# Kernel optimization log

Hardware: AMD Instinct MI355X
Metric: run time of the kernel (lower is better)

The kernel has to match this reference:

```python
import jax, jax.numpy as jnp
import numpy as np
from jax import lax

B, S, D, NH, K = 4, 2048, 1024, 16, 3
EPS = 1e-6


def custom_layernorm(x, gamma, beta):
    # torch-style: std with ddof=1, eps added to std (not var)
    mean = jnp.mean(x, axis=-1, keepdims=True)
    var = jnp.sum((x - mean) ** 2, axis=-1, keepdims=True) / (x.shape[-1] - 1)
    std = jnp.sqrt(var)
    return gamma * ((x - mean) / (std + EPS)) + beta


def setup_inputs() -> dict:
    key = jax.random.key(0)
    ks = jax.random.split(key, 10)
    s = 1.0 / np.sqrt(D)
    return {
        "x": jax.random.normal(ks[0], (B, S, D), jnp.float32),
        "Wq": jax.random.normal(ks[1], (D, D), jnp.float32) * s,
        "bq": jax.random.normal(ks[2], (D,), jnp.float32) * 0.02,
        "Wk": jax.random.normal(ks[3], (D, D), jnp.float32) * s,
        "Wv": jax.random.normal(ks[4], (D, D), jnp.float32) * s,
        "bv": jax.random.normal(ks[5], (D,), jnp.float32) * 0.02,
        "conv_w": jax.random.normal(ks[6], (D, D // NH, K), jnp.float32) * (1.0 / np.sqrt((D // NH) * K)),
        "conv_b": jax.random.normal(ks[7], (D,), jnp.float32) * 0.02,
        "gamma": jnp.ones((D,), jnp.float32),
        "beta": jnp.zeros((D,), jnp.float32),
        "Wo": jax.random.normal(ks[8], (D, D), jnp.float32) * s,
        "bo": jax.random.normal(ks[9], (D,), jnp.float32) * 0.02,
    }


def reference(x, Wq, bq, Wk, Wv, bv, conv_w, conv_b, gamma, beta, Wo, bo):
    d = x.shape[-1]
    groups = d // conv_w.shape[1]
    pad = conv_w.shape[2] // 2

    q = x @ Wq + bq
    k = x @ Wk  # key has no bias
    v = x @ Wv + bv

    # grouped conv1d over sequence dim (NCW layout)
    xc = jnp.transpose(x, (0, 2, 1))  # [B, D, S]
    conv_out = lax.conv_general_dilated(
        xc, conv_w, window_strides=(1,), padding=[(pad, pad)],
        feature_group_count=groups,
        dimension_numbers=("NCH", "OIH", "NCH"),
    ) + conv_b[None, :, None]
    conv_out = jnp.transpose(conv_out, (0, 2, 1))  # [B, S, D]
    conv_out = custom_layernorm(conv_out, gamma, beta)  # dropout = identity (eval)

    scale = 1.0 / jnp.sqrt(jnp.asarray(d, x.dtype))
    scores = jnp.einsum("bqd,bkd->bqk", q, k) * scale  # [B, S, S]
    attn = jax.nn.softmax(scores, axis=-1)
    attention_out = jnp.einsum("bqk,bkd->bqd", attn, v)

    combined = custom_layernorm(conv_out + attention_out, gamma, beta)
    return combined @ Wo + bo + x
```

## Files before the change

### kernel.cpp

```cpp
#include <hip/hip_runtime.h>
#include <cstdint>


#define DEV __device__ __forceinline__

typedef unsigned short u16;
typedef __attribute__((ext_vector_type(8))) short bf16x8;
typedef __attribute__((ext_vector_type(4))) float f32x4;

static const int Sn = 2048, Dn = 1024;

DEV float bf2f(u16 u) { union { unsigned int i; float f; } w; w.i = ((unsigned int)u) << 16; return w.f; }
DEV u16 f2bf(float f) {
  union { float f; unsigned int i; } w; w.f = f;
  unsigned int x = w.i;
  return (u16)((x + 0x7FFFu + ((x >> 16) & 1u)) >> 16);
}

DEV void gload_lds16(const u16* gsrc, u16* lds_dst) {
  __builtin_amdgcn_global_load_lds(
      (const __attribute__((address_space(1))) void*)gsrc,
      (__attribute__((address_space(3))) void*)lds_dst,
      16, 0, 0);
}

DEV float block_allreduce_sum(float v, float* red, int tid) {
  #pragma unroll
  for (int o = 32; o > 0; o >>= 1) v += __shfl_down(v, o, 64);
  __syncthreads();
  if ((tid & 63) == 0) red[tid >> 6] = v;
  __syncthreads();
  return red[0] + red[1] + red[2] + red[3];
}

DEV float block_allreduce_max(float v, float* red, int tid) {
  #pragma unroll
  for (int o = 32; o > 0; o >>= 1) v = fmaxf(v, __shfl_down(v, o, 64));
  __syncthreads();
  if ((tid & 63) == 0) red[tid >> 6] = v;
  __syncthreads();
  return fmaxf(fmaxf(red[0], red[1]), fmaxf(red[2], red[3]));
}

__global__ __launch_bounds__(256)
void cvt_f32_bf16(const float* __restrict__ s, u16* __restrict__ d, int n) {
  int i = (blockIdx.x * 256 + threadIdx.x) * 4;
  if (i >= n) return;
  float4 v = *(const float4*)&s[i];
  ushort4 o;
  o.x = f2bf(v.x); o.y = f2bf(v.y); o.z = f2bf(v.z); o.w = f2bf(v.w);
  *(ushort4*)&d[i] = o;
}

__global__ __launch_bounds__(256)
void transpose_cvt4(const float* __restrict__ w0, const float* __restrict__ w1,
                    const float* __restrict__ w2, const float* __restrict__ w3,
                    u16* __restrict__ dst_base) {
  __shared__ u16 sm[64][68];
  int z = blockIdx.z;
  const float* src = (z == 0) ? w0 : (z == 1) ? w1 : (z == 2) ? w2 : w3;
  u16* dst = dst_base + (size_t)z * 1048576u;
  int i0 = blockIdx.y << 6, j0 = blockIdx.x << 6;
  int tid = threadIdx.x, tx = tid & 15, r0 = tid >> 4;
  #pragma unroll
  for (int rr = r0; rr < 64; rr += 16) {
    float4 v = *(const float4*)&src[(long)(i0 + rr) * 1024 + j0 + tx * 4];
    sm[rr][tx*4+0] = f2bf(v.x); sm[rr][tx*4+1] = f2bf(v.y);
    sm[rr][tx*4+2] = f2bf(v.z); sm[rr][tx*4+3] = f2bf(v.w);
  }
  __syncthreads();
  #pragma unroll
  for (int cc = r0; cc < 64; cc += 16) {
    ushort4 o;
    o.x = sm[tx*4+0][cc]; o.y = sm[tx*4+1][cc];
    o.z = sm[tx*4+2][cc]; o.w = sm[tx*4+3][cc];
    *(ushort4*)&dst[(long)(j0 + cc) * 1024 + i0 + tx * 4] = o;
  }
}

__global__ __launch_bounds__(256)
void transpose_u16(const u16* __restrict__ src, u16* __restrict__ dst,
                   int src_ld, int dst_ld, long sbs, long dbs) {
  __shared__ u16 sm[64][68];
  const u16* s = src + (long)blockIdx.z * sbs;
  u16* d = dst + (long)blockIdx.z * dbs;
  int i0 = blockIdx.y << 6, j0 = blockIdx.x << 6;
  int tid = threadIdx.x, tx = tid & 15, r0 = tid >> 4;
  #pragma unroll
  for (int rr = r0; rr < 64; rr += 16) {
    ushort4 v = *(const ushort4*)&s[(long)(i0 + rr) * src_ld + j0 + tx * 4];
    sm[rr][tx*4+0] = v.x; sm[rr][tx*4+1] = v.y; sm[rr][tx*4+2] = v.z; sm[rr][tx*4+3] = v.w;
  }
  __syncthreads();
  #pragma unroll
  for (int cc = r0; cc < 64; cc += 16) {
    ushort4 o;
    o.x = sm[tx*4+0][cc]; o.y = sm[tx*4+1][cc];
    o.z = sm[tx*4+2][cc]; o.w = sm[tx*4+3][cc];
    *(ushort4*)&d[(long)(j0 + cc) * dst_ld + i0 + tx * 4] = o;
  }
}

__global__ void concat_bias(const float* __restrict__ bq, const float* __restrict__ bv,
                            float* __restrict__ qb) {
  int j = blockIdx.x * 256 + threadIdx.x;
  if (j >= 3072) return;
  float v = 0.0f;
  if (j < 1024) v = bq[j];
  else if (j >= 2048) v = bv[j - 2048];
  qb[j] = v;
}

__global__ void conv_w_prep(const float* __restrict__ w, u16* __restrict__ wt) {
  int oc = blockIdx.x;
  int k = threadIdx.x;
  int t = k >> 6, i = k & 63;
  wt[oc * 192 + k] = f2bf(w[oc * 192 + i * 3 + t]);
}

template<typename CT>
__global__ __launch_bounds__(256, 2)
void gemm_nt(const u16* __restrict__ A, const u16* __restrict__ A2, long Abs, int lda,
             const u16* __restrict__ B, long Bbs, int ldb,
             CT* __restrict__ C, CT* __restrict__ C2, long Cbs, int ldc,
             int zsplit, int K, float scale,
             const float* __restrict__ bias, int bias_bs,
             const float* __restrict__ res, long Rbs, int ldr) {
  __shared__ u16 sA[128 * 32];
  __shared__ u16 sB[128 * 32];
  int tid = threadIdx.x;
  int lane = tid & 63, wv = tid >> 6;
  int quad = lane >> 4, lm = lane & 15;
  int wr = wv >> 1, wc = wv & 1;
  long m0 = (long)blockIdx.x * 128, n0 = (long)blockIdx.y * 128;
  int z = blockIdx.z;
  if (z >= zsplit) { A = A2 + (long)(z - zsplit) * Abs; C = C2 + (long)(z - zsplit) * Cbs; }
  else             { A = A  + (long)z * Abs;            C = C  + (long)z * Cbs; }
  B += (long)z * Bbs;
  if (res) res += (long)z * Rbs;

  f32x4 acc[4][4] = {};

  int srow = wv * 16 + (lane >> 2);
  int sch = (lane & 3) * 8;
  const u16* Ap = A + (m0 + srow) * (long)lda + sch;
  const u16* Bp = B + (n0 + srow) * (long)ldb + sch;
  u16* lA = &sA[wv * 16 * 32];
  u16* lB = &sB[wv * 16 * 32];

  for (int k0 = 0; k0 < K; k0 += 32) {
    gload_lds16(Ap + k0, lA);
    gload_lds16(Ap + 64 * (long)lda + k0, lA + 64 * 32);
    gload_lds16(Bp + k0, lB);
    gload_lds16(Bp + 64 * (long)ldb + k0, lB + 64 * 32);
    __syncthreads();
    bf16x8 af[4], bfr[4];
    #pragma unroll
    for (int mi = 0; mi < 4; mi++)
      af[mi] = *(const bf16x8*)&sA[(wr * 64 + mi * 16 + lm) * 32 + quad * 8];
    #pragma unroll
    for (int ni = 0; ni < 4; ni++)
      bfr[ni] = *(const bf16x8*)&sB[(wc * 64 + ni * 16 + lm) * 32 + quad * 8];
    #pragma unroll
    for (int mi = 0; mi < 4; mi++)
      #pragma unroll
      for (int ni = 0; ni < 4; ni++)
        acc[mi][ni] = __builtin_amdgcn_mfma_f32_16x16x32_bf16(af[mi], bfr[ni], acc[mi][ni], 0, 0, 0);
    __syncthreads();
  }

  #pragma unroll
  for (int mi = 0; mi < 4; mi++) {
    #pragma unroll
    for (int ni = 0; ni < 4; ni++) {
      int col = (int)n0 + wc * 64 + ni * 16 + lm;
      float bv = bias ? bias[(long)z * bias_bs + col] : 0.0f;
      #pragma unroll
      for (int r = 0; r < 4; r++) {
        long rowg = m0 + wr * 64 + mi * 16 + quad * 4 + r;
        float v = acc[mi][ni][r] * scale + bv;
        if (res) v += res[rowg * (long)ldr + col];
        if constexpr (sizeof(CT) == 2) C[rowg * (long)ldc + col] = f2bf(v);
        else                           C[rowg * (long)ldc + col] = v;
      }
    }
  }
}

__global__ __launch_bounds__(256)
void conv_mfma(const u16* __restrict__ xb, const u16* __restrict__ wt,
               const float* __restrict__ cb, u16* __restrict__ out) {
  __shared__ u16 sx[130][72];
  int s0 = blockIdx.x * 128;
  int g = blockIdx.y;
  int b = blockIdx.z;
  int tid = threadIdx.x, lane = tid & 63, wv = tid >> 6;
  int quad = lane >> 4, lm = lane & 15;

  for (int idx = tid; idx < 130 * 16; idx += 256) {
    int r = idx >> 4, c4 = (idx & 15) * 4;
    int s = s0 - 1 + r;
    ushort4 v;
    if (s >= 0 && s < Sn) v = *(const ushort4*)&xb[((long)b * Sn + s) * Dn + g * 64 + c4];
    else { v.x = 0; v.y = 0; v.z = 0; v.w = 0; }
    *(ushort4*)&sx[r][c4] = v;
  }
  __syncthreads();

  f32x4 acc[2][4] = {};
  const u16* wg = wt + (long)g * 64 * 192;
  #pragma unroll
  for (int ks = 0; ks < 6; ks++) {
    int t = ks >> 1;
    int i0 = (ks & 1) * 32 + quad * 8;
    bf16x8 a0 = *(const bf16x8*)&sx[wv * 32 + lm + t][i0];
    bf16x8 a1 = *(const bf16x8*)&sx[wv * 32 + 16 + lm + t][i0];
    #pragma unroll
    for (int nf = 0; nf < 4; nf++) {
      bf16x8 bf = *(const bf16x8*)&wg[(nf * 16 + lm) * 192 + ks * 32 + quad * 8];
      acc[0][nf] = __builtin_amdgcn_mfma_f32_16x16x32_bf16(a0, bf, acc[0][nf], 0, 0, 0);
      acc[1][nf] = __builtin_amdgcn_mfma_f32_16x16x32_bf16(a1, bf, acc[1][nf], 0, 0, 0);
    }
  }
  #pragma unroll
  for (int mi = 0; mi < 2; mi++) {
    #pragma unroll
    for (int nf = 0; nf < 4; nf++) {
      int col = g * 64 + nf * 16 + lm;
      float bias = cb[col];
      #pragma unroll
      for (int r = 0; r < 4; r++) {
        int row = wv * 32 + mi * 16 + quad * 4 + r;
        out[((long)b * Sn + s0 + row) * Dn + col] = f2bf(acc[mi][nf][r] + bias);
      }
    }
  }
}

__global__ __launch_bounds__(256)
void ln_kernel(const u16* __restrict__ a, const u16* __restrict__ b2,
               const float* __restrict__ gamma, const float* __restrict__ beta,
               u16* __restrict__ out) {
  __shared__ float red[4];
  long row = blockIdx.x;
  int tid = threadIdx.x;
  long base = row * Dn + tid * 4;
  ushort4 av = *(const ushort4*)&a[base];
  float v0 = bf2f(av.x), v1 = bf2f(av.y), v2 = bf2f(av.z), v3 = bf2f(av.w);
  if (b2) {
    ushort4 bv4 = *(const ushort4*)&b2[base];
    v0 += bf2f(bv4.x); v1 += bf2f(bv4.y); v2 += bf2f(bv4.z); v3 += bf2f(bv4.w);
  }
  float s = block_allreduce_sum(v0 + v1 + v2 + v3, red, tid);
  float mean = s * (1.0f / 1024.0f);
  float d0 = v0 - mean, d1 = v1 - mean, d2 = v2 - mean, d3 = v3 - mean;
  float sq = block_allreduce_sum(d0 * d0 + d1 * d1 + d2 * d2 + d3 * d3, red, tid);
  float inv = 1.0f / (sqrtf(sq * (1.0f / 1023.0f)) + 1e-6f);
  float4 gv = *(const float4*)&gamma[tid * 4];
  float4 bev = *(const float4*)&beta[tid * 4];
  ushort4 o;
  o.x = f2bf(gv.x * d0 * inv + bev.x);
  o.y = f2bf(gv.y * d1 * inv + bev.y);
  o.z = f2bf(gv.z * d2 * inv + bev.z);
  o.w = f2bf(gv.w * d3 * inv + bev.w);
  *(ushort4*)&out[base] = o;
}

__global__ __launch_bounds__(256)
void softmax_bf16(u16* __restrict__ pa, u16* __restrict__ pb, int rowsplit) {
  __shared__ float red[4];
  long row = blockIdx.x;
  u16* p = (row < rowsplit) ? pa + row * 2048 : pb + (row - rowsplit) * 2048;
  int tid = threadIdx.x;
  ushort4 a = *(const ushort4*)&p[tid * 8];
  ushort4 b = *(const ushort4*)&p[tid * 8 + 4];
  float f0 = bf2f(a.x), f1 = bf2f(a.y), f2 = bf2f(a.z), f3 = bf2f(a.w);
  float f4 = bf2f(b.x), f5 = bf2f(b.y), f6 = bf2f(b.z), f7 = bf2f(b.w);
  float m = fmaxf(fmaxf(fmaxf(f0, f1), fmaxf(f2, f3)),
                  fmaxf(fmaxf(f4, f5), fmaxf(f6, f7)));
  m = block_allreduce_max(m, red, tid);
  float e0 = __expf(f0 - m), e1 = __expf(f1 - m), e2 = __expf(f2 - m), e3 = __expf(f3 - m);
  float e4 = __expf(f4 - m), e5 = __expf(f5 - m), e6 = __expf(f6 - m), e7 = __expf(f7 - m);
  float s = block_allreduce_sum(e0 + e1 + e2 + e3 + e4 + e5 + e6 + e7, red, tid);
  float inv = 1.0f / s;
  ushort4 o1, o2;
  o1.x = f2bf(e0 * inv); o1.y = f2bf(e1 * inv); o1.z = f2bf(e2 * inv); o1.w = f2bf(e3 * inv);
  o2.x = f2bf(e4 * inv); o2.y = f2bf(e5 * inv); o2.z = f2bf(e6 * inv); o2.w = f2bf(e7 * inv);
  *(ushort4*)&p[tid * 8] = o1;
  *(ushort4*)&p[tid * 8 + 4] = o2;
}

static const size_t OFF_WT    = 0;
static const size_t OFF_QKVB  = 8ull << 20;
static const size_t OFF_WCONV = (8ull << 20) + (64 << 10);
static const size_t OFF_Q     = 9ull << 20;
static const size_t OFF_K     = 25ull << 20;
static const size_t OFF_V     = 41ull << 20;
static const size_t OFF_PW    = 57ull << 20;

extern "C" void kernel_launch(void* const* d_in, const int* in_sizes, int n_in,
                              void* d_out, int out_size, void* d_ws, size_t ws_size,
                              hipStream_t stream) {
  const float* x     = (const float*)d_in[0];
  const float* Wq    = (const float*)d_in[1];
  const float* bq    = (const float*)d_in[2];
  const float* Wk    = (const float*)d_in[3];
  const float* Wv    = (const float*)d_in[4];
  const float* bv    = (const float*)d_in[5];
  const float* cw    = (const float*)d_in[6];
  const float* cb    = (const float*)d_in[7];
  const float* gamma = (const float*)d_in[8];
  const float* beta  = (const float*)d_in[9];
  const float* Wo    = (const float*)d_in[10];
  const float* bo    = (const float*)d_in[11];
  float* out = (float*)d_out;
  char* ws = (char*)d_ws;

  u16*   wT    = (u16*)(ws + OFF_WT);
  float* qkvb  = (float*)(ws + OFF_QKVB);
  u16*   wconv = (u16*)(ws + OFF_WCONV);
  u16*   Qb    = (u16*)(ws + OFF_Q);
  u16*   Kb    = (u16*)(ws + OFF_K);
  u16*   Vb    = (u16*)(ws + OFF_V);
  u16*   Pw    = (u16*)(ws + OFF_PW);
  u16*   xb    = (u16*)d_out;
  u16*   Pd    = (u16*)d_out;
  u16*   vt    = (u16*)d_out + 8388608;
  u16*   conv  = Vb;
  u16*   attn  = Qb;
  u16*   combined = Kb;
  const long PBS = (long)Sn * Sn;

  dim3 tb(256);

  transpose_cvt4<<<dim3(16, 16, 4), tb, 0, stream>>>(Wq, Wk, Wv, Wo, wT);
  concat_bias<<<dim3(12), tb, 0, stream>>>(bq, bv, qkvb);
  conv_w_prep<<<dim3(1024), dim3(192), 0, stream>>>(cw, wconv);
  cvt_f32_bf16<<<dim3(8192), tb, 0, stream>>>(x, xb, 8388608);

  gemm_nt<u16><<<dim3(64, 8, 3), tb, 0, stream>>>(
      xb, nullptr, 0, 1024, wT, 1048576, 1024, Qb, (u16*)nullptr, 8388608, 1024,
      99, 1024, 1.0f, qkvb, 1024, nullptr, 0, 0);
  transpose_u16<<<dim3(16, 32, 4), tb, 0, stream>>>(
      Vb, vt, 1024, 2048, (long)Sn * Dn, (long)Dn * Sn);
  conv_mfma<<<dim3(16, 16, 4), tb, 0, stream>>>(xb, wconv, cb, conv);
  ln_kernel<<<dim3(8192), tb, 0, stream>>>(conv, nullptr, gamma, beta, conv);

  if (ws_size >= (73ull << 20)) {
    gemm_nt<u16><<<dim3(16, 16, 4), tb, 0, stream>>>(
        Qb, Qb + 2 * (long)Sn * Dn, (long)Sn * Dn, 1024,
        Kb, (long)Sn * Dn, 1024,
        Pd, Pw, PBS, 2048,
        2, 1024, 0.03125f, nullptr, 0, nullptr, 0, 0);
    softmax_bf16<<<dim3(8192), tb, 0, stream>>>(Pd, Pw, 4096);
    gemm_nt<u16><<<dim3(16, 8, 4), tb, 0, stream>>>(
        Pd, Pw, PBS, 2048,
        vt, (long)Dn * Sn, 2048,
        attn, attn + 2 * (long)Sn * Dn, (long)Sn * Dn, 1024,
        2, 2048, 1.0f, nullptr, 0, nullptr, 0, 0);
  } else {
    for (int c = 0; c < 2; c++) {
      long off = (long)c * 2 * Sn * Dn;
      gemm_nt<u16><<<dim3(16, 16, 2), tb, 0, stream>>>(
          Qb + off, nullptr, (long)Sn * Dn, 1024, Kb + off, (long)Sn * Dn, 1024,
          Pd, (u16*)nullptr, PBS, 2048,
          99, 1024, 0.03125f, nullptr, 0, nullptr, 0, 0);
      softmax_bf16<<<dim3(4096), tb, 0, stream>>>(Pd, Pd, 4096);
      gemm_nt<u16><<<dim3(16, 8, 2), tb, 0, stream>>>(
          Pd, nullptr, PBS, 2048, vt + off, (long)Dn * Sn, 2048,
          attn + off, (u16*)nullptr, (long)Sn * Dn, 1024,
          99, 2048, 1.0f, nullptr, 0, nullptr, 0, 0);
    }
  }

  ln_kernel<<<dim3(8192), tb, 0, stream>>>(conv, attn, gamma, beta, combined);
  gemm_nt<float><<<dim3(64, 8, 1), tb, 0, stream>>>(
      combined, nullptr, 0, 1024, wT + 3u * 1048576u, 0, 1024,
      out, (float*)nullptr, 0, 1024,
      99, 1024, 1.0f, bo, 0, x, 0, 1024);
}
```

Baseline: 383.4 us.

## Merge prep kernels, merge conv with V transpose, and load two K-slices per GEMM sync

New measurement: 359.4 us. 1.07x faster.

```diff
diff --git a/kernel.cpp b/kernel.cpp
--- a/kernel.cpp
+++ b/kernel.cpp
@@ -43,79 +43,57 @@
 }
 
 __global__ __launch_bounds__(256)
-void cvt_f32_bf16(const float* __restrict__ s, u16* __restrict__ d, int n) {
-  int i = (blockIdx.x * 256 + threadIdx.x) * 4;
-  if (i >= n) return;
-  float4 v = *(const float4*)&s[i];
-  ushort4 o;
-  o.x = f2bf(v.x); o.y = f2bf(v.y); o.z = f2bf(v.z); o.w = f2bf(v.w);
-  *(ushort4*)&d[i] = o;
-}
-
-__global__ __launch_bounds__(256)
-void transpose_cvt4(const float* __restrict__ w0, const float* __restrict__ w1,
-                    const float* __restrict__ w2, const float* __restrict__ w3,
-                    u16* __restrict__ dst_base) {
+void prep_all(const float* __restrict__ Wq, const float* __restrict__ Wk,
+              const float* __restrict__ Wv, const float* __restrict__ Wo,
+              u16* __restrict__ wT,
+              const float* __restrict__ bq, const float* __restrict__ bv,
+              float* __restrict__ qkvb,
+              const float* __restrict__ cw, u16* __restrict__ wconv,
+              const float* __restrict__ x, u16* __restrict__ xb) {
   __shared__ u16 sm[64][68];
-  int z = blockIdx.z;
-  const float* src = (z == 0) ? w0 : (z == 1) ? w1 : (z == 2) ? w2 : w3;
-  u16* dst = dst_base + (size_t)z * 1048576u;
-  int i0 = blockIdx.y << 6, j0 = blockIdx.x << 6;
-  int tid = threadIdx.x, tx = tid & 15, r0 = tid >> 4;
-  #pragma unroll
-  for (int rr = r0; rr < 64; rr += 16) {
-    float4 v = *(const float4*)&src[(long)(i0 + rr) * 1024 + j0 + tx * 4];
-    sm[rr][tx*4+0] = f2bf(v.x); sm[rr][tx*4+1] = f2bf(v.y);
-    sm[rr][tx*4+2] = f2bf(v.z); sm[rr][tx*4+3] = f2bf(v.w);
-  }
-  __syncthreads();
-  #pragma unroll
-  for (int cc = r0; cc < 64; cc += 16) {
+  int blk = blockIdx.x;
+  int tid = threadIdx.x;
+  if (blk < 1024) {
+    int w = blk >> 8, t = blk & 255;
+    const float* src = (w == 0) ? Wq : (w == 1) ? Wk : (w == 2) ? Wv : Wo;
+    u16* dst = wT + (size_t)w * 1048576u;
+    int i0 = (t >> 4) << 6, j0 = (t & 15) << 6;
+    int tx = tid & 15, r0 = tid >> 4;
+    #pragma unroll
+    for (int rr = r0; rr < 64; rr += 16) {
+      float4 v = *(const float4*)&src[(long)(i0 + rr) * 1024 + j0 + tx * 4];
+      sm[rr][tx*4+0] = f2bf(v.x); sm[rr][tx*4+1] = f2bf(v.y);
+      sm[rr][tx*4+2] = f2bf(v.z); sm[rr][tx*4+3] = f2bf(v.w);
+    }
+    __syncthreads();
+    #pragma unroll
+    for (int cc = r0; cc < 64; cc += 16) {
+      ushort4 o;
+      o.x = sm[tx*4+0][cc]; o.y = sm[tx*4+1][cc];
+      o.z = sm[tx*4+2][cc]; o.w = sm[tx*4+3][cc];
+      *(ushort4*)&dst[(long)(j0 + cc) * 1024 + i0 + tx * 4] = o;
+    }
+  } else if (blk < 1040) {
+    int oc0 = (blk - 1024) * 64;
+    for (int idx = tid; idx < 64 * 192; idx += 256) {
+      int oc = oc0 + idx / 192; int k = idx % 192;
+      int t = k >> 6, i = k & 63;
+      wconv[(long)oc * 192 + k] = f2bf(cw[(long)oc * 192 + i * 3 + t]);
+    }
+  } else if (blk == 1040) {
+    for (int j = tid; j < 3072; j += 256) {
+      float v = 0.0f;
+      if (j < 1024) v = bq[j];
+      else if (j >= 2048) v = bv[j - 2048];
+      qkvb[j] = v;
+    }
+  } else {
+    int i = (blk - 1041) * 1024 + tid * 4;
+    float4 v = *(const float4*)&x[i];
     ushort4 o;
-    o.x = sm[tx*4+0][cc]; o.y = sm[tx*4+1][cc];
-    o.z = sm[tx*4+2][cc]; o.w = sm[tx*4+3][cc];
-    *(ushort4*)&dst[(long)(j0 + cc) * 1024 + i0 + tx * 4] = o;
-  }
-}
-
-__global__ __launch_bounds__(256)
-void transpose_u16(const u16* __restrict__ src, u16* __restrict__ dst,
-                   int src_ld, int dst_ld, long sbs, long dbs) {
-  __shared__ u16 sm[64][68];
-  const u16* s = src + (long)blockIdx.z * sbs;
-  u16* d = dst + (long)blockIdx.z * dbs;
-  int i0 = blockIdx.y << 6, j0 = blockIdx.x << 6;
-  int tid = threadIdx.x, tx = tid & 15, r0 = tid >> 4;
-  #pragma unroll
-  for (int rr = r0; rr < 64; rr += 16) {
-    ushort4 v = *(const ushort4*)&s[(long)(i0 + rr) * src_ld + j0 + tx * 4];
-    sm[rr][tx*4+0] = v.x; sm[rr][tx*4+1] = v.y; sm[rr][tx*4+2] = v.z; sm[rr][tx*4+3] = v.w;
-  }
-  __syncthreads();
-  #pragma unroll
-  for (int cc = r0; cc < 64; cc += 16) {
-    ushort4 o;
-    o.x = sm[tx*4+0][cc]; o.y = sm[tx*4+1][cc];
-    o.z = sm[tx*4+2][cc]; o.w = sm[tx*4+3][cc];
-    *(ushort4*)&d[(long)(j0 + cc) * dst_ld + i0 + tx * 4] = o;
-  }
-}
-
-__global__ void concat_bias(const float* __restrict__ bq, const float* __restrict__ bv,
-                            float* __restrict__ qb) {
-  int j = blockIdx.x * 256 + threadIdx.x;
-  if (j >= 3072) return;
-  float v = 0.0f;
-  if (j < 1024) v = bq[j];
-  else if (j >= 2048) v = bv[j - 2048];
-  qb[j] = v;
-}
-
-__global__ void conv_w_prep(const float* __restrict__ w, u16* __restrict__ wt) {
-  int oc = blockIdx.x;
-  int k = threadIdx.x;
-  int t = k >> 6, i = k & 63;
-  wt[oc * 192 + k] = f2bf(w[oc * 192 + i * 3 + t]);
+    o.x = f2bf(v.x); o.y = f2bf(v.y); o.z = f2bf(v.z); o.w = f2bf(v.w);
+    *(ushort4*)&xb[i] = o;
+  }
 }
 
 template<typename CT>
@@ -126,8 +104,8 @@
              int zsplit, int K, float scale,
              const float* __restrict__ bias, int bias_bs,
              const float* __restrict__ res, long Rbs, int ldr) {
-  __shared__ u16 sA[128 * 32];
-  __shared__ u16 sB[128 * 32];
+  __shared__ u16 sA[2][128 * 32];
+  __shared__ u16 sB[2][128 * 32];
   int tid = threadIdx.x;
   int lane = tid & 63, wv = tid >> 6;
   int quad = lane >> 4, lm = lane & 15;
@@ -145,27 +123,33 @@
   int sch = (lane & 3) * 8;
   const u16* Ap = A + (m0 + srow) * (long)lda + sch;
   const u16* Bp = B + (n0 + srow) * (long)ldb + sch;
-  u16* lA = &sA[wv * 16 * 32];
-  u16* lB = &sB[wv * 16 * 32];
-
-  for (int k0 = 0; k0 < K; k0 += 32) {
-    gload_lds16(Ap + k0, lA);
-    gload_lds16(Ap + 64 * (long)lda + k0, lA + 64 * 32);
-    gload_lds16(Bp + k0, lB);
-    gload_lds16(Bp + 64 * (long)ldb + k0, lB + 64 * 32);
-    __syncthreads();
-    bf16x8 af[4], bfr[4];
-    #pragma unroll
-    for (int mi = 0; mi < 4; mi++)
-      af[mi] = *(const bf16x8*)&sA[(wr * 64 + mi * 16 + lm) * 32 + quad * 8];
-    #pragma unroll
-    for (int ni = 0; ni < 4; ni++)
-      bfr[ni] = *(const bf16x8*)&sB[(wc * 64 + ni * 16 + lm) * 32 + quad * 8];
-    #pragma unroll
-    for (int mi = 0; mi < 4; mi++)
+  const int lofs = wv * 16 * 32;
+
+  for (int k0 = 0; k0 < K; k0 += 64) {
+    #pragma unroll
+    for (int h = 0; h < 2; h++) {
+      int kh = k0 + h * 32;
+      gload_lds16(Ap + kh, &sA[h][lofs]);
+      gload_lds16(Ap + 64 * (long)lda + kh, &sA[h][lofs + 64 * 32]);
+      gload_lds16(Bp + kh, &sB[h][lofs]);
+      gload_lds16(Bp + 64 * (long)ldb + kh, &sB[h][lofs + 64 * 32]);
+    }
+    __syncthreads();
+    #pragma unroll
+    for (int h = 0; h < 2; h++) {
+      bf16x8 af[4], bfr[4];
+      #pragma unroll
+      for (int mi = 0; mi < 4; mi++)
+        af[mi] = *(const bf16x8*)&sA[h][(wr * 64 + mi * 16 + lm) * 32 + quad * 8];
       #pragma unroll
       for (int ni = 0; ni < 4; ni++)
-        acc[mi][ni] = __builtin_amdgcn_mfma_f32_16x16x32_bf16(af[mi], bfr[ni], acc[mi][ni], 0, 0, 0);
+        bfr[ni] = *(const bf16x8*)&sB[h][(wc * 64 + ni * 16 + lm) * 32 + quad * 8];
+      #pragma unroll
+      for (int mi = 0; mi < 4; mi++)
+        #pragma unroll
+        for (int ni = 0; ni < 4; ni++)
+          acc[mi][ni] = __builtin_amdgcn_mfma_f32_16x16x32_bf16(af[mi], bfr[ni], acc[mi][ni], 0, 0, 0);
+    }
     __syncthreads();
   }
 
@@ -188,51 +172,76 @@
 }
 
 __global__ __launch_bounds__(256)
-void conv_mfma(const u16* __restrict__ xb, const u16* __restrict__ wt,
-               const float* __restrict__ cb, u16* __restrict__ out) {
-  __shared__ u16 sx[130][72];
-  int s0 = blockIdx.x * 128;
-  int g = blockIdx.y;
-  int b = blockIdx.z;
-  int tid = threadIdx.x, lane = tid & 63, wv = tid >> 6;
-  int quad = lane >> 4, lm = lane & 15;
-
-  for (int idx = tid; idx < 130 * 16; idx += 256) {
-    int r = idx >> 4, c4 = (idx & 15) * 4;
-    int s = s0 - 1 + r;
-    ushort4 v;
-    if (s >= 0 && s < Sn) v = *(const ushort4*)&xb[((long)b * Sn + s) * Dn + g * 64 + c4];
-    else { v.x = 0; v.y = 0; v.z = 0; v.w = 0; }
-    *(ushort4*)&sx[r][c4] = v;
-  }
-  __syncthreads();
-
-  f32x4 acc[2][4] = {};
-  const u16* wg = wt + (long)g * 64 * 192;
-  #pragma unroll
-  for (int ks = 0; ks < 6; ks++) {
-    int t = ks >> 1;
-    int i0 = (ks & 1) * 32 + quad * 8;
-    bf16x8 a0 = *(const bf16x8*)&sx[wv * 32 + lm + t][i0];
-    bf16x8 a1 = *(const bf16x8*)&sx[wv * 32 + 16 + lm + t][i0];
-    #pragma unroll
-    for (int nf = 0; nf < 4; nf++) {
-      bf16x8 bf = *(const bf16x8*)&wg[(nf * 16 + lm) * 192 + ks * 32 + quad * 8];
-      acc[0][nf] = __builtin_amdgcn_mfma_f32_16x16x32_bf16(a0, bf, acc[0][nf], 0, 0, 0);
-      acc[1][nf] = __builtin_amdgcn_mfma_f32_16x16x32_bf16(a1, bf, acc[1][nf], 0, 0, 0);
-    }
-  }
-  #pragma unroll
-  for (int mi = 0; mi < 2; mi++) {
-    #pragma unroll
-    for (int nf = 0; nf < 4; nf++) {
-      int col = g * 64 + nf * 16 + lm;
-      float bias = cb[col];
-      #pragma unroll
-      for (int r = 0; r < 4; r++) {
-        int row = wv * 32 + mi * 16 + quad * 4 + r;
-        out[((long)b * Sn + s0 + row) * Dn + col] = f2bf(acc[mi][nf][r] + bias);
+void mid_all(const u16* __restrict__ xb, const u16* __restrict__ wt,
+             const float* __restrict__ cb, u16* __restrict__ convo,
+             const u16* __restrict__ Vb, u16* __restrict__ vt) {
+  __shared__ u16 smem[9360];
+  int blk = blockIdx.x;
+  int tid = threadIdx.x;
+  if (blk < 1024) {
+    u16 (*sx)[72] = (u16(*)[72])smem;
+    int s0 = (blk & 15) * 128;
+    int g = (blk >> 4) & 15;
+    int b = blk >> 8;
+    int lane = tid & 63, wv = tid >> 6;
+    int quad = lane >> 4, lm = lane & 15;
+    for (int idx = tid; idx < 130 * 16; idx += 256) {
+      int r = idx >> 4, c4 = (idx & 15) * 4;
+      int s = s0 - 1 + r;
+      ushort4 v;
+      if (s >= 0 && s < Sn) v = *(const ushort4*)&xb[((long)b * Sn + s) * Dn + g * 64 + c4];
+      else { v.x = 0; v.y = 0; v.z = 0; v.w = 0; }
+      *(ushort4*)&sx[r][c4] = v;
+    }
+    __syncthreads();
+    f32x4 acc[2][4] = {};
+    const u16* wg = wt + (long)g * 64 * 192;
+    #pragma unroll
+    for (int ks = 0; ks < 6; ks++) {
+      int t = ks >> 1;
+      int i0 = (ks & 1) * 32 + quad * 8;
+      bf16x8 a0 = *(const bf16x8*)&sx[wv * 32 + lm + t][i0];
+      bf16x8 a1 = *(const bf16x8*)&sx[wv * 32 + 16 + lm + t][i0];
+      #pragma unroll
+      for (int nf = 0; nf < 4; nf++) {
+        bf16x8 bf = *(const bf16x8*)&wg[(nf * 16 + lm) * 192 + ks * 32 + quad * 8];
+        acc[0][nf] = __builtin_amdgcn_mfma_f32_16x16x32_bf16(a0, bf, acc[0][nf], 0, 0, 0);
+        acc[1][nf] = __builtin_amdgcn_mfma_f32_16x16x32_bf16(a1, bf, acc[1][nf], 0, 0, 0);
       }
+    }
+    #pragma unroll
+    for (int mi = 0; mi < 2; mi++) {
+      #pragma unroll
+      for (int nf = 0; nf < 4; nf++) {
+        int col = g * 64 + nf * 16 + lm;
+        float bias = cb[col];
+        #pragma unroll
+        for (int r = 0; r < 4; r++) {
+          int row = wv * 32 + mi * 16 + quad * 4 + r;
+          convo[((long)b * Sn + s0 + row) * Dn + col] = f2bf(acc[mi][nf][r] + bias);
+        }
+      }
+    }
+  } else {
+    u16 (*sm)[68] = (u16(*)[68])smem;
+    int t = blk - 1024;
+    int b = t >> 9, r = t & 511;
+    int j0 = (r & 15) << 6, i0 = ((r >> 4) & 31) << 6;
+    const u16* s = Vb + (long)b * Sn * Dn;
+    u16* d = vt + (long)b * Dn * Sn;
+    int tx = tid & 15, r0 = tid >> 4;
+    #pragma unroll
+    for (int rr = r0; rr < 64; rr += 16) {
+      ushort4 v = *(const ushort4*)&s[(long)(i0 + rr) * 1024 + j0 + tx * 4];
+      sm[rr][tx*4+0] = v.x; sm[rr][tx*4+1] = v.y; sm[rr][tx*4+2] = v.z; sm[rr][tx*4+3] = v.w;
+    }
+    __syncthreads();
+    #pragma unroll
+    for (int cc = r0; cc < 64; cc += 16) {
+      ushort4 o;
+      o.x = sm[tx*4+0][cc]; o.y = sm[tx*4+1][cc];
+      o.z = sm[tx*4+2][cc]; o.w = sm[tx*4+3][cc];
+      *(ushort4*)&d[(long)(j0 + cc) * 2048 + i0 + tx * 4] = o;
     }
   }
 }
@@ -333,17 +342,12 @@
 
   dim3 tb(256);
 
-  transpose_cvt4<<<dim3(16, 16, 4), tb, 0, stream>>>(Wq, Wk, Wv, Wo, wT);
-  concat_bias<<<dim3(12), tb, 0, stream>>>(bq, bv, qkvb);
-  conv_w_prep<<<dim3(1024), dim3(192), 0, stream>>>(cw, wconv);
-  cvt_f32_bf16<<<dim3(8192), tb, 0, stream>>>(x, xb, 8388608);
-
+  prep_all<<<dim3(9233), tb, 0, stream>>>(Wq, Wk, Wv, Wo, wT, bq, bv, qkvb,
+                                          cw, wconv, x, xb);
   gemm_nt<u16><<<dim3(64, 8, 3), tb, 0, stream>>>(
       xb, nullptr, 0, 1024, wT, 1048576, 1024, Qb, (u16*)nullptr, 8388608, 1024,
       99, 1024, 1.0f, qkvb, 1024, nullptr, 0, 0);
-  transpose_u16<<<dim3(16, 32, 4), tb, 0, stream>>>(
-      Vb, vt, 1024, 2048, (long)Sn * Dn, (long)Dn * Sn);
-  conv_mfma<<<dim3(16, 16, 4), tb, 0, stream>>>(xb, wconv, cb, conv);
+  mid_all<<<dim3(3072), tb, 0, stream>>>(xb, wconv, cb, conv, Vb, vt);
   ln_kernel<<<dim3(8192), tb, 0, stream>>>(conv, nullptr, gamma, beta, conv);
 
   if (ws_size >= (73ull << 20)) {
```
